# Optimization experiments

Hardware: AMD Instinct MI355X
Metric: run time of the kernel (lower is better)

The kernel has to match this reference:

```python
import jax, jax.numpy as jnp
import numpy as np

N, E, F_IN, HID, OUT, HEADS, NG = 40000, 640000, 64, 128, 64, 4, 64
EPS = 1e-5

def setup_inputs() -> dict:
    key = jax.random.key(0)
    ks = jax.random.split(key, 32)
    d = {}
    d['x'] = jax.random.normal(ks[0], (N, F_IN), dtype=jnp.float32)
    d['edge_index'] = jax.random.randint(ks[1], (2, E), 0, N, dtype=jnp.int64)
    d['batch'] = jnp.sort(jax.random.randint(ks[2], (N,), 0, NG, dtype=jnp.int64))
    fins = [F_IN, HID, HID]
    for i in range(3):
        kk = jax.random.split(ks[3 + i], 6)
        fin = fins[i]
        d[f'W{i}'] = jax.random.normal(kk[0], (fin, HEADS * HID), dtype=jnp.float32) / np.sqrt(fin)
        d[f'as{i}'] = jax.random.normal(kk[1], (HEADS, HID), dtype=jnp.float32) / np.sqrt(HID)
        d[f'ad{i}'] = jax.random.normal(kk[2], (HEADS, HID), dtype=jnp.float32) / np.sqrt(HID)
        d[f'b{i}'] = jnp.zeros((HID,), dtype=jnp.float32)
        d[f'g{i}'] = jnp.ones((HID,), dtype=jnp.float32) + 0.05 * jax.random.normal(kk[3], (HID,), dtype=jnp.float32)
        d[f'be{i}'] = 0.05 * jax.random.normal(kk[4], (HID,), dtype=jnp.float32)
    d['fc1_w'] = jax.random.normal(ks[10], (HID, HID), dtype=jnp.float32) / np.sqrt(HID)
    d['fc1_b'] = jnp.zeros((HID,), dtype=jnp.float32)
    d['fc2_w'] = jax.random.normal(ks[11], (HID, OUT), dtype=jnp.float32) / np.sqrt(HID)
    d['fc2_b'] = jnp.zeros((OUT,), dtype=jnp.float32)
    return d

def _gat(x, src, dst, W, a_s, a_d, b):
    # PyG GATConv, heads=4, concat=False (mean over heads)
    xh = (x @ W).reshape(N, HEADS, HID)            # [N,H,C]
    s_src = jnp.einsum('nhc,hc->nh', xh, a_s)      # [N,H]
    s_dst = jnp.einsum('nhc,hc->nh', xh, a_d)
    e = jax.nn.leaky_relu(s_src[src] + s_dst[dst], 0.2)   # [Etot,H]
    m = jax.ops.segment_max(e, dst, num_segments=N)
    p = jnp.exp(e - m[dst])
    denom = jax.ops.segment_sum(p, dst, num_segments=N)
    alpha = p / denom[dst]                          # segment softmax over dst
    msg = xh[src] * alpha[:, :, None]               # [Etot,H,C]
    out = jax.ops.segment_sum(msg, dst, num_segments=N)  # [N,H,C]
    return out.mean(axis=1) + b

def _bn_eval(x, g, be):
    # running_mean=0, running_var=1 (eval mode)
    return x * (g / jnp.sqrt(1.0 + EPS)) + be

def reference(x, edge_index, batch, W0, as0, ad0, b0, g0, be0, W1, as1, ad1, b1, g1, be1, W2, as2, ad2, b2, g2, be2, fc1_w, fc1_b, fc2_w, fc2_b):
    loop = jnp.arange(N, dtype=edge_index.dtype)
    src = jnp.concatenate([edge_index[0], loop])   # add_self_loops (PyG default)
    dst = jnp.concatenate([edge_index[1], loop])
    h = x
    params = [(W0, as0, ad0, b0, g0, be0), (W1, as1, ad1, b1, g1, be1), (W2, as2, ad2, b2, g2, be2)]
    for (W, a_s, a_d, b, g, be) in params:
        h = _gat(h, src, dst, W, a_s, a_d, b)
        h = jax.nn.relu(_bn_eval(h, g, be))
        # dropout is identity in eval mode
    sums = jax.ops.segment_sum(h, batch, num_segments=NG)
    cnt = jax.ops.segment_sum(jnp.ones((N,), h.dtype), batch, num_segments=NG)
    pooled = sums / jnp.maximum(cnt, 1.0)[:, None]   # global_mean_pool [NG,HID]
    out = jax.nn.relu(pooled @ fc1_w + fc1_b)
    return out @ fc2_w + fc2_b
```

## Files before the change

### kernel.cpp

```cpp
#include <hip/hip_runtime.h>
#include <hip/hip_fp16.h>
#include <math.h>

#define N_NODES 40000
#define N_EDGES 640000
#define FIN 64
#define HID 128
#define OUTDIM 64
#define HEADS 4
#define NGROUPS 64
#define NCOLS 512

typedef _Float16 half8 __attribute__((ext_vector_type(8)));
typedef float f32x4 __attribute__((ext_vector_type(4)));

__device__ __forceinline__ float lrelu(float x) { return x > 0.f ? x : 0.2f * x; }

__device__ __forceinline__ void wave_lds_fence() {
    asm volatile("s_waitcnt lgkmcnt(0)" ::: "memory");
}

#define PREP_X4   (N_NODES * FIN / 4)
#define PREP_WSWZ 20480
#define PREP_V    2560
__global__ void prep_kernel(const float* __restrict__ x, __half* __restrict__ x16,
                            const float* __restrict__ W0, const float* __restrict__ W1,
                            const float* __restrict__ W2,
                            _Float16* __restrict__ F0, _Float16* __restrict__ F1,
                            _Float16* __restrict__ F2,
                            const float* __restrict__ as0, const float* __restrict__ ad0,
                            const float* __restrict__ as1, const float* __restrict__ ad1,
                            const float* __restrict__ as2, const float* __restrict__ ad2,
                            float* __restrict__ v0, float* __restrict__ v1,
                            float* __restrict__ v2) {
    int id = blockIdx.x * 256 + threadIdx.x;
    if (id < PREP_X4) {
        int i4 = id * 4;
        float4 v = *(const float4*)(x + i4);
        __half2 a = __floats2half2_rn(v.x, v.y);
        __half2 b = __floats2half2_rn(v.z, v.w);
        *(__half2*)(x16 + i4)     = a;
        *(__half2*)(x16 + i4 + 2) = b;
        return;
    }
    id -= PREP_X4;
    if (id < PREP_WSWZ) {
        const float* W; _Float16* F; int Kin;
        if (id < 4096)       { W = W0; F = F0; Kin = FIN; }
        else if (id < 12288) { W = W1; F = F1; Kin = HID; id -= 4096; }
        else                 { W = W2; F = F2; Kin = HID; id -= 12288; }
        int KP = Kin * 4;
        int NKg = KP / 32;
        int lane = id & 63;
        int blob = id >> 6;
        int k0g = blob % NKg;
        int cb  = blob / NKg;
        int col = cb * 16 + (lane & 15);
        int kkb = k0g * 32 + (lane >> 4) * 8;
        half8 v;
        #pragma unroll
        for (int e = 0; e < 8; ++e) {
            int kk = kkb + e;
            int k = kk & (Kin - 1);
            int h = kk / Kin;
            v[e] = (_Float16)(0.25f * W[(size_t)k * NCOLS + h * HID + col]);
        }
        *(half8*)(F + (size_t)blob * 512 + lane * 8) = v;
        return;
    }
    id -= PREP_WSWZ;
    if (id < PREP_V) {
        const float* W; const float* as_; const float* ad_; float* v; int j = id;
        if (j < FIN * 8)              { W = W0; as_ = as0; ad_ = ad0; v = v0; }
        else if (j < (FIN + HID) * 8) { W = W1; as_ = as1; ad_ = ad1; v = v1; j -= FIN * 8; }
        else                          { W = W2; as_ = as2; ad_ = ad2; v = v2; j -= (FIN + HID) * 8; }
        int k = j >> 3, sd = (j >> 2) & 1, h = j & 3;
        const float* av = sd ? ad_ : as_;
        float acc = 0.f;
        for (int c = 0; c < HID; ++c)
            acc += W[(size_t)k * NCOLS + h * HID + c] * av[h * HID + c];
        v[k * 8 + sd * 4 + h] = acc;
    }
}

__global__ void deg_count_kernel(const int* __restrict__ ei, int* deg) {
    int e = blockIdx.x * blockDim.x + threadIdx.x;
    if (e < N_EDGES) atomicAdd(&deg[ei[N_EDGES + e]], 1);
}

__global__ void scan1_kernel(const int* __restrict__ deg, int* offsets, int* partial) {
    __shared__ int buf[256];
    int t = threadIdx.x;
    int i = blockIdx.x * 256 + t;
    int v = (i < N_NODES) ? deg[i] + 1 : 0;
    buf[t] = v;
    __syncthreads();
    for (int off = 1; off < 256; off <<= 1) {
        int y = (t >= off) ? buf[t - off] : 0;
        __syncthreads();
        buf[t] += y;
        __syncthreads();
    }
    if (i < N_NODES) offsets[i] = buf[t] - v;
    if (t == 255) partial[blockIdx.x] = buf[255];
}

__global__ void scan2_kernel(int* partial, int nb) {
    __shared__ int buf[256];
    int t = threadIdx.x;
    int v = (t < nb) ? partial[t] : 0;
    buf[t] = v;
    __syncthreads();
    for (int off = 1; off < 256; off <<= 1) {
        int y = (t >= off) ? buf[t - off] : 0;
        __syncthreads();
        buf[t] += y;
        __syncthreads();
    }
    if (t < nb) partial[t] = buf[t] - v;
}

__global__ void scan3_kernel(int* offsets, int* pos, const int* __restrict__ partial) {
    int i = blockIdx.x * 256 + threadIdx.x;
    if (i < N_NODES) {
        int o = offsets[i] + partial[i >> 8];
        offsets[i] = o;
        pos[i] = o;
    }
    if (i == 0) offsets[N_NODES] = N_EDGES + N_NODES;
}

__global__ void scatter_kernel(const int* __restrict__ ei, int* pos, int* csr_src) {
    int i = blockIdx.x * blockDim.x + threadIdx.x;
    if (i < N_EDGES) {
        int s = ei[i];
        int d = ei[N_EDGES + i];
        csr_src[atomicAdd(&pos[d], 1)] = s;
    } else if (i < N_EDGES + N_NODES) {
        int nn = i - N_EDGES;
        csr_src[atomicAdd(&pos[nn], 1)] = nn;
    }
}

template <int K>
__global__ __launch_bounds__(256) void scores3_kernel(const __half* __restrict__ x,
                                                      const float* __restrict__ v,
                                                      float* __restrict__ ssrc,
                                                      float* __restrict__ sdst) {
    __shared__ float vs[K * 8];
    int t = threadIdx.x;
    for (int i = t; i < K * 8; i += 256) vs[i] = v[i];
    __syncthreads();
    int node = blockIdx.x * 256 + t;
    if (node >= N_NODES) return;
    const __half* xr = x + (size_t)node * K;
    f32x4 as = {0.f, 0.f, 0.f, 0.f};
    f32x4 ad = {0.f, 0.f, 0.f, 0.f};
    #pragma unroll 4
    for (int k0 = 0; k0 < K; k0 += 8) {
        uint4 u = *(const uint4*)(xr + k0);
        __half2* hp = (__half2*)&u;
        #pragma unroll
        for (int q = 0; q < 4; ++q) {
            float2 f = __half22float2(hp[q]);
            int k = k0 + 2 * q;
            as += f.x * *(const f32x4*)&vs[k * 8];
            ad += f.x * *(const f32x4*)&vs[k * 8 + 4];
            as += f.y * *(const f32x4*)&vs[(k + 1) * 8];
            ad += f.y * *(const f32x4*)&vs[(k + 1) * 8 + 4];
        }
    }
    *(f32x4*)(ssrc + node * 4) = as;
    *(f32x4*)(sdst + node * 4) = ad;
}

template <int K>
__global__ __launch_bounds__(256) void aggregate_lin_kernel(const __half* __restrict__ tab16,
                                                            const float* __restrict__ s_src,
                                                            const float* __restrict__ s_dst,
                                                            const int* __restrict__ offsets,
                                                            const int* __restrict__ csr_src,
                                                            __half* __restrict__ agg) {
    constexpr int EPR = (K == 128) ? 4 : 8;
    constexpr int LPE = 64 / EPR;
    int wv = threadIdx.x >> 6;
    int lane = threadIdx.x & 63;
    int n = blockIdx.x * 4 + wv;
    if (n >= N_NODES) return;
    int start = offsets[n], end = offsets[n + 1];
    int deg = end - start;
    const float4 sd = *(const float4*)(s_dst + n * 4);
    int cgrp = lane & (LPE - 1);
    int egoff = lane / LPE;

    __shared__ int   roff[4][72];
    __shared__ float al[4][72][4];

    const char* xb = (const char*)tab16 + cgrp * 16;
    float acc[4][8] = {};

    if (lane < 8) {
        roff[wv][64 + lane] = 0;
        *(f32x4*)&al[wv][64 + lane][0] = f32x4{0.f, 0.f, 0.f, 0.f};
    }

    if (deg <= 64) {
        bool act = lane < deg;
        int src = act ? csr_src[start + lane] : 0;
        float4 ss = *(const float4*)(s_src + src * 4);
        float e0 = act ? lrelu(ss.x + sd.x) : -1e30f;
        float e1 = act ? lrelu(ss.y + sd.y) : -1e30f;
        float e2 = act ? lrelu(ss.z + sd.z) : -1e30f;
        float e3 = act ? lrelu(ss.w + sd.w) : -1e30f;
        float m0 = e0, m1 = e1, m2 = e2, m3 = e3;
        #pragma unroll
        for (int o = 32; o > 0; o >>= 1) {
            m0 = fmaxf(m0, __shfl_xor(m0, o));
            m1 = fmaxf(m1, __shfl_xor(m1, o));
            m2 = fmaxf(m2, __shfl_xor(m2, o));
            m3 = fmaxf(m3, __shfl_xor(m3, o));
        }
        float p0 = __expf(e0 - m0), p1 = __expf(e1 - m1);
        float p2 = __expf(e2 - m2), p3 = __expf(e3 - m3);
        float s0 = p0, s1 = p1, s2 = p2, s3 = p3;
        #pragma unroll
        for (int o = 32; o > 0; o >>= 1) {
            s0 += __shfl_xor(s0, o);
            s1 += __shfl_xor(s1, o);
            s2 += __shfl_xor(s2, o);
            s3 += __shfl_xor(s3, o);
        }
        f32x4 av = {p0 / s0, p1 / s1, p2 / s2, p3 / s3};
        roff[wv][lane] = src * (K * 2);
        *(f32x4*)&al[wv][lane][0] = av;
        wave_lds_fence();

        for (int j = 0; j < deg; j += EPR) {
            int eg = j + egoff;
            f32x4 a4 = *(const f32x4*)&al[wv][eg][0];
            uint4 u = *(const uint4*)(xb + roff[wv][eg]);
            __half2* hp = (__half2*)&u;
            #pragma unroll
            for (int q = 0; q < 4; ++q) {
                float2 f = __half22float2(hp[q]);
                #pragma unroll
                for (int h = 0; h < 4; ++h) {
                    acc[h][2 * q]     += a4[h] * f.x;
                    acc[h][2 * q + 1] += a4[h] * f.y;
                }
            }
        }
    } else {
        float m0 = -1e30f, m1 = -1e30f, m2 = -1e30f, m3 = -1e30f;
        for (int j0 = 0; j0 < deg; j0 += 64) {
            int j = j0 + lane;
            bool act = j < deg;
            int src = act ? csr_src[start + j] : 0;
            float4 ss = *(const float4*)(s_src + src * 4);
            m0 = fmaxf(m0, act ? lrelu(ss.x + sd.x) : -1e30f);
            m1 = fmaxf(m1, act ? lrelu(ss.y + sd.y) : -1e30f);
            m2 = fmaxf(m2, act ? lrelu(ss.z + sd.z) : -1e30f);
            m3 = fmaxf(m3, act ? lrelu(ss.w + sd.w) : -1e30f);
        }
        #pragma unroll
        for (int o = 32; o > 0; o >>= 1) {
            m0 = fmaxf(m0, __shfl_xor(m0, o));
            m1 = fmaxf(m1, __shfl_xor(m1, o));
            m2 = fmaxf(m2, __shfl_xor(m2, o));
            m3 = fmaxf(m3, __shfl_xor(m3, o));
        }
        float s0 = 0.f, s1 = 0.f, s2 = 0.f, s3 = 0.f;
        for (int j0 = 0; j0 < deg; j0 += 64) {
            int j = j0 + lane;
            bool act = j < deg;
            int src = act ? csr_src[start + j] : 0;
            float4 ss = *(const float4*)(s_src + src * 4);
            s0 += act ? __expf(lrelu(ss.x + sd.x) - m0) : 0.f;
            s1 += act ? __expf(lrelu(ss.y + sd.y) - m1) : 0.f;
            s2 += act ? __expf(lrelu(ss.z + sd.z) - m2) : 0.f;
            s3 += act ? __expf(lrelu(ss.w + sd.w) - m3) : 0.f;
        }
        #pragma unroll
        for (int o = 32; o > 0; o >>= 1) {
            s0 += __shfl_xor(s0, o);
            s1 += __shfl_xor(s1, o);
            s2 += __shfl_xor(s2, o);
            s3 += __shfl_xor(s3, o);
        }
        float i0 = 1.f / s0, i1 = 1.f / s1, i2 = 1.f / s2, i3 = 1.f / s3;
        for (int j0 = 0; j0 < deg; j0 += 64) {
            int j = j0 + lane;
            bool act = j < deg;
            int src = act ? csr_src[start + j] : 0;
            float4 ss = *(const float4*)(s_src + src * 4);
            f32x4 av;
            av[0] = act ? __expf(lrelu(ss.x + sd.x) - m0) * i0 : 0.f;
            av[1] = act ? __expf(lrelu(ss.y + sd.y) - m1) * i1 : 0.f;
            av[2] = act ? __expf(lrelu(ss.z + sd.z) - m2) * i2 : 0.f;
            av[3] = act ? __expf(lrelu(ss.w + sd.w) - m3) * i3 : 0.f;
            roff[wv][lane] = act ? src * (K * 2) : 0;
            *(f32x4*)&al[wv][lane][0] = av;
            wave_lds_fence();
            int cend = min(64, deg - j0);
            for (int j2 = 0; j2 < cend; j2 += EPR) {
                int eg = j2 + egoff;
                f32x4 a4 = *(const f32x4*)&al[wv][eg][0];
                uint4 u = *(const uint4*)(xb + roff[wv][eg]);
                __half2* hp = (__half2*)&u;
                #pragma unroll
                for (int q = 0; q < 4; ++q) {
                    float2 f = __half22float2(hp[q]);
                    #pragma unroll
                    for (int h = 0; h < 4; ++h) {
                        acc[h][2 * q]     += a4[h] * f.x;
                        acc[h][2 * q + 1] += a4[h] * f.y;
                    }
                }
            }
            wave_lds_fence();
        }
    }

    #pragma unroll
    for (int stride = LPE; stride < 64; stride <<= 1) {
        #pragma unroll
        for (int h = 0; h < 4; ++h)
            #pragma unroll
            for (int r = 0; r < 8; ++r)
                acc[h][r] += __shfl_xor(acc[h][r], stride);
    }
    if (lane < LPE) {
        _Float16* ap = (_Float16*)agg + (size_t)n * (4 * K);
        #pragma unroll
        for (int h = 0; h < 4; ++h) {
            half8 v;
            #pragma unroll
            for (int r = 0; r < 8; ++r) v[r] = (_Float16)acc[h][r];
            *(half8*)(ap + h * K + cgrp * 8) = v;
        }
    }
}

template <int KP, bool SCORES>
__global__ __launch_bounds__(256) void gemm_ep_kernel(const __half* __restrict__ agg,
                                                      const _Float16* __restrict__ Wf,
                                                      const float* __restrict__ bias,
                                                      const float* __restrict__ gamma,
                                                      const float* __restrict__ beta,
                                                      const float* __restrict__ vtab_next,
                                                      __half* __restrict__ h16,
                                                      float* __restrict__ ssrc,
                                                      float* __restrict__ sdst) {
    __shared__ _Float16 As[32][KP + 8];
    __shared__ _Float16 tb[32][136];
    __shared__ float bn_s[3][HID];
    __shared__ float vs[SCORES ? HID * 8 : 8];
    int bm = blockIdx.x * 32;
    int t = threadIdx.x;
    int lane = t & 63;
    int w = t >> 6;
    int wm = w >> 1, wn = w & 1;
    int lr = lane & 15;
    int lk = (lane >> 4) * 8;
    int lg = lane >> 4;

    if (t < HID) {
        bn_s[0][t] = bias[t];
        bn_s[1][t] = gamma[t] * rsqrtf(1.f + 1e-5f);
        bn_s[2][t] = beta[t];
    }
    if (SCORES)
        for (int i = t; i < HID * 8; i += 256) vs[i] = vtab_next[i];
    {
        int row = t >> 3;
        #pragma unroll
        for (int it = 0; it < KP / 64; ++it) {
            int k8 = (t & 7) * 8 + it * 64;
            uint4 av = *(const uint4*)((const _Float16*)agg + (size_t)(bm + row) * KP + k8);
            *(uint4*)&As[row][k8] = av;
        }
    }
    __syncthreads();

    constexpr int NKg = KP / 32;
    f32x4 acc[4] = {};
    #pragma unroll
    for (int k0g = 0; k0g < NKg; ++k0g) {
        half8 af = *(const half8*)&As[wm * 16 + lr][k0g * 32 + lk];
        #pragma unroll
        for (int nn = 0; nn < 4; ++nn) {
            int cb = wn * 4 + nn;
            half8 bf = *(const half8*)(Wf + ((size_t)(cb * NKg + k0g) << 9) + lane * 8);
            acc[nn] = __builtin_amdgcn_mfma_f32_16x16x32_f16(af, bf, acc[nn], 0, 0, 0);
        }
    }

    #pragma unroll
    for (int nn = 0; nn < 4; ++nn) {
        int col = wn * 64 + nn * 16 + lr;
        float b = bn_s[0][col], g = bn_s[1][col], be = bn_s[2][col];
        #pragma unroll
        for (int r = 0; r < 4; ++r) {
            float o = acc[nn][r] + b;
            o = o * g + be;
            tb[wm * 16 + lg * 4 + r][col] = (_Float16)fmaxf(o, 0.f);
        }
    }
    __syncthreads();

    {
        int row = t >> 3;
        int c0 = (t & 7) * 16;
        half8 v0 = *(const half8*)&tb[row][c0];
        half8 v1 = *(const half8*)&tb[row][c0 + 8];
        _Float16* cp = (_Float16*)h16 + (size_t)(bm + row) * HID + c0;
        *(half8*)(cp)     = v0;
        *(half8*)(cp + 8) = v1;
    }

    if (SCORES) {
        int node = t >> 3, j = t & 7;
        float sacc = 0.f;
        #pragma unroll 2
        for (int k0 = 0; k0 < HID; k0 += 8) {
            half8 hv = *(const half8*)&tb[node][k0];
            #pragma unroll
            for (int e = 0; e < 8; ++e)
                sacc += (float)hv[e] * vs[(k0 + e) * 8 + j];
        }
        if (j < 4) ssrc[(bm + node) * 4 + j] = sacc;
        else       sdst[(bm + node) * 4 + (j - 4)] = sacc;
    }
}

__global__ __launch_bounds__(128) void pool_kernel(const __half* __restrict__ h,
                                                   const int* __restrict__ batch,
                                                   float* pooled, float* counts) {
    int t = threadIdx.x;
    int which = t >> 6;
    int c2 = (t & 63) * 2;
    int n0 = blockIdx.x * 256 + which;
    int n1 = min(blockIdx.x * 256 + 256, N_NODES);
    if (n0 >= N_NODES) return;
    int cg = batch[n0];
    float a0 = 0.f, a1 = 0.f, cnt = 0.f;
    for (int n = n0; n < n1; n += 2) {
        int g = batch[n];
        if (g != cg) {
            atomicAdd(&pooled[cg * HID + c2], a0);
            atomicAdd(&pooled[cg * HID + c2 + 1], a1);
            if ((t & 63) == 0) atomicAdd(&counts[cg], cnt);
            a0 = 0.f; a1 = 0.f; cnt = 0.f; cg = g;
        }
        uint u = *(const uint*)(h + (size_t)n * HID + c2);
        __half2 hh = *(__half2*)&u;
        float2 f = __half22float2(hh);
        a0 += f.x; a1 += f.y; cnt += 1.f;
    }
    atomicAdd(&pooled[cg * HID + c2], a0);
    atomicAdd(&pooled[cg * HID + c2 + 1], a1);
    if ((t & 63) == 0) atomicAdd(&counts[cg], cnt);
}

__global__ __launch_bounds__(128) void head_kernel(const float* __restrict__ pooled,
                                                   const float* __restrict__ counts,
                                                   const float* __restrict__ fc1_w,
                                                   const float* __restrict__ fc1_b,
                                                   const float* __restrict__ fc2_w,
                                                   const float* __restrict__ fc2_b,
                                                   float* __restrict__ out) {
    int gI = blockIdx.x;
    int t = threadIdx.x;
    __shared__ float p[HID], hb[HID];
    p[t] = pooled[gI * HID + t] / fmaxf(counts[gI], 1.f);
    __syncthreads();
    float a = fc1_b[t];
    #pragma unroll 4
    for (int k = 0; k < HID; ++k) a += p[k] * fc1_w[k * HID + t];
    hb[t] = fmaxf(a, 0.f);
    __syncthreads();
    if (t < OUTDIM) {
        float o = fc2_b[t];
        #pragma unroll 4
        for (int k = 0; k < HID; ++k) o += hb[k] * fc2_w[k * OUTDIM + t];
        out[gI * OUTDIM + t] = o;
    }
}

extern "C" void kernel_launch(void* const* d_in, const int* in_sizes, int n_in,
                              void* d_out, int out_size, void* d_ws, size_t ws_size,
                              hipStream_t stream) {
    const float* x     = (const float*)d_in[0];
    const int*   ei    = (const int*)d_in[1];
    const int*   batch = (const int*)d_in[2];
    const float* W[3]  = {(const float*)d_in[3],  (const float*)d_in[9],  (const float*)d_in[15]};
    const float* As[3] = {(const float*)d_in[4],  (const float*)d_in[10], (const float*)d_in[16]};
    const float* Ad[3] = {(const float*)d_in[5],  (const float*)d_in[11], (const float*)d_in[17]};
    const float* Bb[3] = {(const float*)d_in[6],  (const float*)d_in[12], (const float*)d_in[18]};
    const float* Gg[3] = {(const float*)d_in[7],  (const float*)d_in[13], (const float*)d_in[19]};
    const float* Be[3] = {(const float*)d_in[8],  (const float*)d_in[14], (const float*)d_in[20]};
    const float* fc1_w = (const float*)d_in[21];
    const float* fc1_b = (const float*)d_in[22];
    const float* fc2_w = (const float*)d_in[23];
    const float* fc2_b = (const float*)d_in[24];

    char* ws = (char*)d_ws;
    size_t off = 0;
    auto alloc = [&](size_t bytes) {
        void* p = ws + off;
        off = (off + bytes + 255) & ~(size_t)255;
        return p;
    };
    __half* agg    = (__half*)alloc((size_t)N_NODES * NCOLS * 2);
    __half* x16    = (__half*)alloc((size_t)N_NODES * FIN * 2);
    __half* h16    = (__half*)alloc((size_t)N_NODES * HID * 2);
    _Float16* Wf[3];
    Wf[0] = (_Float16*)alloc((size_t)(4 * FIN) * HID * 2);
    Wf[1] = (_Float16*)alloc((size_t)(4 * HID) * HID * 2);
    Wf[2] = (_Float16*)alloc((size_t)(4 * HID) * HID * 2);
    float* vtab[3];
    vtab[0] = (float*)alloc((size_t)FIN * 8 * 4);
    vtab[1] = (float*)alloc((size_t)HID * 8 * 4);
    vtab[2] = (float*)alloc((size_t)HID * 8 * 4);
    float* ssrc    = (float*)alloc((size_t)N_NODES * HEADS * 4);
    float* sdst    = (float*)alloc((size_t)N_NODES * HEADS * 4);
    int*   deg     = (int*)alloc((size_t)N_NODES * 4);
    int*   offsets = (int*)alloc((size_t)(N_NODES + 1) * 4);
    int*   pos     = (int*)alloc((size_t)N_NODES * 4);
    int*   partial = (int*)alloc((size_t)256 * 4);
    int*   csr     = (int*)alloc((size_t)(N_EDGES + N_NODES) * 4);
    float* pooled  = (float*)alloc((size_t)NGROUPS * HID * 4 + (size_t)NGROUPS * 4);
    float* counts  = pooled + (size_t)NGROUPS * HID;

    const int PREP_TOTAL = PREP_X4 + PREP_WSWZ + PREP_V;
    prep_kernel<<<(PREP_TOTAL + 255) / 256, 256, 0, stream>>>(
        x, x16, W[0], W[1], W[2], Wf[0], Wf[1], Wf[2],
        As[0], Ad[0], As[1], Ad[1], As[2], Ad[2], vtab[0], vtab[1], vtab[2]);

    const int NB = (N_NODES + 255) / 256;
    hipMemsetAsync(deg, 0, (size_t)N_NODES * 4, stream);
    deg_count_kernel<<<(N_EDGES + 255) / 256, 256, 0, stream>>>(ei, deg);
    scan1_kernel<<<NB, 256, 0, stream>>>(deg, offsets, partial);
    scan2_kernel<<<1, 256, 0, stream>>>(partial, NB);
    scan3_kernel<<<NB, 256, 0, stream>>>(offsets, pos, partial);
    scatter_kernel<<<(N_EDGES + N_NODES + 255) / 256, 256, 0, stream>>>(ei, pos, csr);

    scores3_kernel<64><<<NB, 256, 0, stream>>>(x16, vtab[0], ssrc, sdst);

    aggregate_lin_kernel<64><<<(N_NODES + 3) / 4, 256, 0, stream>>>(
        x16, ssrc, sdst, offsets, csr, agg);
    gemm_ep_kernel<256, true><<<N_NODES / 32, 256, 0, stream>>>(
        agg, Wf[0], Bb[0], Gg[0], Be[0], vtab[1], h16, ssrc, sdst);

    aggregate_lin_kernel<128><<<(N_NODES + 3) / 4, 256, 0, stream>>>(
        h16, ssrc, sdst, offsets, csr, agg);
    gemm_ep_kernel<512, true><<<N_NODES / 32, 256, 0, stream>>>(
        agg, Wf[1], Bb[1], Gg[1], Be[1], vtab[2], h16, ssrc, sdst);

    aggregate_lin_kernel<128><<<(N_NODES + 3) / 4, 256, 0, stream>>>(
        h16, ssrc, sdst, offsets, csr, agg);
    gemm_ep_kernel<512, false><<<N_NODES / 32, 256, 0, stream>>>(
        agg, Wf[2], Bb[2], Gg[2], Be[2], nullptr, h16, nullptr, nullptr);

    hipMemsetAsync(pooled, 0, (size_t)NGROUPS * HID * 4 + (size_t)NGROUPS * 4, stream);
    pool_kernel<<<(N_NODES + 255) / 256, 128, 0, stream>>>(h16, batch, pooled, counts);
    head_kernel<<<NGROUPS, 128, 0, stream>>>(pooled, counts, fc1_w, fc1_b, fc2_w, fc2_b,
                                             (float*)d_out);
}
```

Baseline: 391.4 us.

## Fuse attention aggregation and per-layer GEMM epilogue into one kernel

Merges the aggregate and GEMM+BN+ReLU+scores kernels into a single 512-thread kernel per GAT layer. Each wave aggregates four destination nodes directly into an LDS tile, then the block runs MFMA GEMM on that tile. This removes the global round trip of the 40000x512 fp16 aggregate buffer and one launch per layer. Ping-pong buffers for h and scores avoid read/write hazards between blocks. The trade-off is a larger LDS footprint per block, which may lower occupancy, and the GEMM phase must wait for the slowest wave's gather.

```diff
diff --git a/kernel.cpp b/kernel.cpp
--- a/kernel.cpp
+++ b/kernel.cpp
@@ -174,136 +174,98 @@
     *(f32x4*)(sdst + node * 4) = ad;
 }
 
-template <int K>
-__global__ __launch_bounds__(256) void aggregate_lin_kernel(const __half* __restrict__ tab16,
-                                                            const float* __restrict__ s_src,
-                                                            const float* __restrict__ s_dst,
-                                                            const int* __restrict__ offsets,
-                                                            const int* __restrict__ csr_src,
-                                                            __half* __restrict__ agg) {
+template <int K, bool SCORES>
+__global__ __launch_bounds__(512) void fused_layer_kernel(
+        const __half* __restrict__ tab16,
+        const float* __restrict__ s_src,
+        const float* __restrict__ s_dst,
+        const int* __restrict__ offsets,
+        const int* __restrict__ csr_src,
+        const _Float16* __restrict__ Wf,
+        const float* __restrict__ bias,
+        const float* __restrict__ gamma,
+        const float* __restrict__ beta,
+        const float* __restrict__ vtab_next,
+        __half* __restrict__ h16out,
+        float* __restrict__ ssrc_o,
+        float* __restrict__ sdst_o) {
+    constexpr int KP = 4 * K;
     constexpr int EPR = (K == 128) ? 4 : 8;
     constexpr int LPE = 64 / EPR;
-    int wv = threadIdx.x >> 6;
-    int lane = threadIdx.x & 63;
-    int n = blockIdx.x * 4 + wv;
-    if (n >= N_NODES) return;
-    int start = offsets[n], end = offsets[n + 1];
-    int deg = end - start;
-    const float4 sd = *(const float4*)(s_dst + n * 4);
+    constexpr int NKg = KP / 32;
+
+    __shared__ _Float16 As[32][KP + 8];
+    __shared__ __align__(16) char uali[11520];
+    __shared__ float bn_s[3][HID];
+    __shared__ float vs[SCORES ? HID * 8 : 8];
+
+    int (*roff)[72]    = (int(*)[72])uali;
+    float (*al)[72][4] = (float(*)[72][4])(uali + 8 * 72 * 4);
+    _Float16 (*tb)[136] = (_Float16(*)[136])uali;
+
+    int t = threadIdx.x;
+    int lane = t & 63;
+    int wv = t >> 6;
+    int bm = blockIdx.x * 32;
+
+    if (t < HID) {
+        bn_s[0][t] = bias[t];
+        bn_s[1][t] = gamma[t] * rsqrtf(1.f + 1e-5f);
+        bn_s[2][t] = beta[t];
+    }
+    if (SCORES)
+        for (int i = t; i < HID * 8; i += 512) vs[i] = vtab_next[i];
+
     int cgrp = lane & (LPE - 1);
     int egoff = lane / LPE;
-
-    __shared__ int   roff[4][72];
-    __shared__ float al[4][72][4];
-
     const char* xb = (const char*)tab16 + cgrp * 16;
-    float acc[4][8] = {};
 
     if (lane < 8) {
         roff[wv][64 + lane] = 0;
         *(f32x4*)&al[wv][64 + lane][0] = f32x4{0.f, 0.f, 0.f, 0.f};
     }
 
-    if (deg <= 64) {
-        bool act = lane < deg;
-        int src = act ? csr_src[start + lane] : 0;
-        float4 ss = *(const float4*)(s_src + src * 4);
-        float e0 = act ? lrelu(ss.x + sd.x) : -1e30f;
-        float e1 = act ? lrelu(ss.y + sd.y) : -1e30f;
-        float e2 = act ? lrelu(ss.z + sd.z) : -1e30f;
-        float e3 = act ? lrelu(ss.w + sd.w) : -1e30f;
-        float m0 = e0, m1 = e1, m2 = e2, m3 = e3;
-        #pragma unroll
-        for (int o = 32; o > 0; o >>= 1) {
-            m0 = fmaxf(m0, __shfl_xor(m0, o));
-            m1 = fmaxf(m1, __shfl_xor(m1, o));
-            m2 = fmaxf(m2, __shfl_xor(m2, o));
-            m3 = fmaxf(m3, __shfl_xor(m3, o));
-        }
-        float p0 = __expf(e0 - m0), p1 = __expf(e1 - m1);
-        float p2 = __expf(e2 - m2), p3 = __expf(e3 - m3);
-        float s0 = p0, s1 = p1, s2 = p2, s3 = p3;
-        #pragma unroll
-        for (int o = 32; o > 0; o >>= 1) {
-            s0 += __shfl_xor(s0, o);
-            s1 += __shfl_xor(s1, o);
-            s2 += __shfl_xor(s2, o);
-            s3 += __shfl_xor(s3, o);
-        }
-        f32x4 av = {p0 / s0, p1 / s1, p2 / s2, p3 / s3};
-        roff[wv][lane] = src * (K * 2);
-        *(f32x4*)&al[wv][lane][0] = av;
-        wave_lds_fence();
-
-        for (int j = 0; j < deg; j += EPR) {
-            int eg = j + egoff;
-            f32x4 a4 = *(const f32x4*)&al[wv][eg][0];
-            uint4 u = *(const uint4*)(xb + roff[wv][eg]);
-            __half2* hp = (__half2*)&u;
+    for (int i = 0; i < 4; ++i) {
+        int nl = wv * 4 + i;
+        int n = bm + nl;
+        int start = offsets[n], end = offsets[n + 1];
+        int deg = end - start;
+        const float4 sd = *(const float4*)(s_dst + n * 4);
+        float acc[4][8] = {};
+
+        if (deg <= 64) {
+            bool act = lane < deg;
+            int src = act ? csr_src[start + lane] : 0;
+            float4 ss = *(const float4*)(s_src + src * 4);
+            float e0 = act ? lrelu(ss.x + sd.x) : -1e30f;
+            float e1 = act ? lrelu(ss.y + sd.y) : -1e30f;
+            float e2 = act ? lrelu(ss.z + sd.z) : -1e30f;
+            float e3 = act ? lrelu(ss.w + sd.w) : -1e30f;
+            float m0 = e0, m1 = e1, m2 = e2, m3 = e3;
             #pragma unroll
-            for (int q = 0; q < 4; ++q) {
-                float2 f = __half22float2(hp[q]);
-                #pragma unroll
-                for (int h = 0; h < 4; ++h) {
-                    acc[h][2 * q]     += a4[h] * f.x;
-                    acc[h][2 * q + 1] += a4[h] * f.y;
-                }
-            }
-        }
-    } else {
-        float m0 = -1e30f, m1 = -1e30f, m2 = -1e30f, m3 = -1e30f;
-        for (int j0 = 0; j0 < deg; j0 += 64) {
-            int j = j0 + lane;
-            bool act = j < deg;
-            int src = act ? csr_src[start + j] : 0;
-            float4 ss = *(const float4*)(s_src + src * 4);
-            m0 = fmaxf(m0, act ? lrelu(ss.x + sd.x) : -1e30f);
-            m1 = fmaxf(m1, act ? lrelu(ss.y + sd.y) : -1e30f);
-            m2 = fmaxf(m2, act ? lrelu(ss.z + sd.z) : -1e30f);
-            m3 = fmaxf(m3, act ? lrelu(ss.w + sd.w) : -1e30f);
-        }
-        #pragma unroll
-        for (int o = 32; o > 0; o >>= 1) {
-            m0 = fmaxf(m0, __shfl_xor(m0, o));
-            m1 = fmaxf(m1, __shfl_xor(m1, o));
-            m2 = fmaxf(m2, __shfl_xor(m2, o));
-            m3 = fmaxf(m3, __shfl_xor(m3, o));
-        }
-        float s0 = 0.f, s1 = 0.f, s2 = 0.f, s3 = 0.f;
-        for (int j0 = 0; j0 < deg; j0 += 64) {
-            int j = j0 + lane;
-            bool act = j < deg;
-            int src = act ? csr_src[start + j] : 0;
-            float4 ss = *(const float4*)(s_src + src * 4);
-            s0 += act ? __expf(lrelu(ss.x + sd.x) - m0) : 0.f;
-            s1 += act ? __expf(lrelu(ss.y + sd.y) - m1) : 0.f;
-            s2 += act ? __expf(lrelu(ss.z + sd.z) - m2) : 0.f;
-            s3 += act ? __expf(lrelu(ss.w + sd.w) - m3) : 0.f;
-        }
-        #pragma unroll
-        for (int o = 32; o > 0; o >>= 1) {
-            s0 += __shfl_xor(s0, o);
-            s1 += __shfl_xor(s1, o);
-            s2 += __shfl_xor(s2, o);
-            s3 += __shfl_xor(s3, o);
-        }
-        float i0 = 1.f / s0, i1 = 1.f / s1, i2 = 1.f / s2, i3 = 1.f / s3;
-        for (int j0 = 0; j0 < deg; j0 += 64) {
-            int j = j0 + lane;
-            bool act = j < deg;
-            int src = act ? csr_src[start + j] : 0;
-            float4 ss = *(const float4*)(s_src + src * 4);
-            f32x4 av;
-            av[0] = act ? __expf(lrelu(ss.x + sd.x) - m0) * i0 : 0.f;
-            av[1] = act ? __expf(lrelu(ss.y + sd.y) - m1) * i1 : 0.f;
-            av[2] = act ? __expf(lrelu(ss.z + sd.z) - m2) * i2 : 0.f;
-            av[3] = act ? __expf(lrelu(ss.w + sd.w) - m3) * i3 : 0.f;
-            roff[wv][lane] = act ? src * (K * 2) : 0;
+            for (int o = 32; o > 0; o >>= 1) {
+                m0 = fmaxf(m0, __shfl_xor(m0, o));
+                m1 = fmaxf(m1, __shfl_xor(m1, o));
+                m2 = fmaxf(m2, __shfl_xor(m2, o));
+                m3 = fmaxf(m3, __shfl_xor(m3, o));
+            }
+            float p0 = __expf(e0 - m0), p1 = __expf(e1 - m1);
+            float p2 = __expf(e2 - m2), p3 = __expf(e3 - m3);
+            float s0 = p0, s1 = p1, s2 = p2, s3 = p3;
+            #pragma unroll
+            for (int o = 32; o > 0; o >>= 1) {
+                s0 += __shfl_xor(s0, o);
+                s1 += __shfl_xor(s1, o);
+                s2 += __shfl_xor(s2, o);
+                s3 += __shfl_xor(s3, o);
+            }
+            f32x4 av = {p0 / s0, p1 / s1, p2 / s2, p3 / s3};
+            roff[wv][lane] = src * (K * 2);
             *(f32x4*)&al[wv][lane][0] = av;
             wave_lds_fence();
-            int cend = min(64, deg - j0);
-            for (int j2 = 0; j2 < cend; j2 += EPR) {
-                int eg = j2 + egoff;
+
+            for (int j = 0; j < deg; j += EPR) {
+                int eg = j + egoff;
                 f32x4 a4 = *(const f32x4*)&al[wv][eg][0];
                 uint4 u = *(const uint4*)(xb + roff[wv][eg]);
                 __half2* hp = (__half2*)&u;
@@ -317,91 +279,121 @@
                     }
                 }
             }
-            wave_lds_fence();
-        }
-    }
-
-    #pragma unroll
-    for (int stride = LPE; stride < 64; stride <<= 1) {
+        } else {
+            float m0 = -1e30f, m1 = -1e30f, m2 = -1e30f, m3 = -1e30f;
+            for (int j0 = 0; j0 < deg; j0 += 64) {
+                int j = j0 + lane;
+                bool act = j < deg;
+                int src = act ? csr_src[start + j] : 0;
+                float4 ss = *(const float4*)(s_src + src * 4);
+                m0 = fmaxf(m0, act ? lrelu(ss.x + sd.x) : -1e30f);
+                m1 = fmaxf(m1, act ? lrelu(ss.y + sd.y) : -1e30f);
+                m2 = fmaxf(m2, act ? lrelu(ss.z + sd.z) : -1e30f);
+                m3 = fmaxf(m3, act ? lrelu(ss.w + sd.w) : -1e30f);
+            }
+            #pragma unroll
+            for (int o = 32; o > 0; o >>= 1) {
+                m0 = fmaxf(m0, __shfl_xor(m0, o));
+                m1 = fmaxf(m1, __shfl_xor(m1, o));
+                m2 = fmaxf(m2, __shfl_xor(m2, o));
+                m3 = fmaxf(m3, __shfl_xor(m3, o));
+            }
+            float s0 = 0.f, s1 = 0.f, s2 = 0.f, s3 = 0.f;
+            for (int j0 = 0; j0 < deg; j0 += 64) {
+                int j = j0 + lane;
+                bool act = j < deg;
+                int src = act ? csr_src[start + j] : 0;
+                float4 ss = *(const float4*)(s_src + src * 4);
+                s0 += act ? __expf(lrelu(ss.x + sd.x) - m0) : 0.f;
+                s1 += act ? __expf(lrelu(ss.y + sd.y) - m1) : 0.f;
+                s2 += act ? __expf(lrelu(ss.z + sd.z) - m2) : 0.f;
+                s3 += act ? __expf(lrelu(ss.w + sd.w) - m3) : 0.f;
+            }
+            #pragma unroll
+            for (int o = 32; o > 0; o >>= 1) {
+                s0 += __shfl_xor(s0, o);
+                s1 += __shfl_xor(s1, o);
+                s2 += __shfl_xor(s2, o);
+                s3 += __shfl_xor(s3, o);
+            }
+            float i0 = 1.f / s0, i1 = 1.f / s1, i2 = 1.f / s2, i3 = 1.f / s3;
+            for (int j0 = 0; j0 < deg; j0 += 64) {
+                int j = j0 + lane;
+                bool act = j < deg;
+                int src = act ? csr_src[start + j] : 0;
+                float4 ss = *(const float4*)(s_src + src * 4);
+                f32x4 av;
+                av[0] = act ? __expf(lrelu(ss.x + sd.x) - m0) * i0 : 0.f;
+                av[1] = act ? __expf(lrelu(ss.y + sd.y) - m1) * i1 : 0.f;
+                av[2] = act ? __expf(lrelu(ss.z + sd.z) - m2) * i2 : 0.f;
+                av[3] = act ? __expf(lrelu(ss.w + sd.w) - m3) * i3 : 0.f;
+                roff[wv][lane] = act ? src * (K * 2) : 0;
+                *(f32x4*)&al[wv][lane][0] = av;
+                wave_lds_fence();
+                int cend = min(64, deg - j0);
+                for (int j2 = 0; j2 < cend; j2 += EPR) {
+                    int eg = j2 + egoff;
+                    f32x4 a4 = *(const f32x4*)&al[wv][eg][0];
+                    uint4 u = *(const uint4*)(xb + roff[wv][eg]);
+                    __half2* hp = (__half2*)&u;
+                    #pragma unroll
+                    for (int q = 0; q < 4; ++q) {
+                        float2 f = __half22float2(hp[q]);
+                        #pragma unroll
+                        for (int h = 0; h < 4; ++h) {
+                            acc[h][2 * q]     += a4[h] * f.x;
+                            acc[h][2 * q + 1] += a4[h] * f.y;
+                        }
+                    }
+                }
+                wave_lds_fence();
+            }
+        }
+
         #pragma unroll
-        for (int h = 0; h < 4; ++h)
+        for (int stride = LPE; stride < 64; stride <<= 1) {
             #pragma unroll
-            for (int r = 0; r < 8; ++r)
-                acc[h][r] += __shfl_xor(acc[h][r], stride);
-    }
-    if (lane < LPE) {
-        _Float16* ap = (_Float16*)agg + (size_t)n * (4 * K);
-        #pragma unroll
-        for (int h = 0; h < 4; ++h) {
-            half8 v;
+            for (int h = 0; h < 4; ++h)
+                #pragma unroll
+                for (int r = 0; r < 8; ++r)
+                    acc[h][r] += __shfl_xor(acc[h][r], stride);
+        }
+        if (lane < LPE) {
             #pragma unroll
-            for (int r = 0; r < 8; ++r) v[r] = (_Float16)acc[h][r];
-            *(half8*)(ap + h * K + cgrp * 8) = v;
-        }
-    }
-}
-
-template <int KP, bool SCORES>
-__global__ __launch_bounds__(256) void gemm_ep_kernel(const __half* __restrict__ agg,
-                                                      const _Float16* __restrict__ Wf,
-                                                      const float* __restrict__ bias,
-                                                      const float* __restrict__ gamma,
-                                                      const float* __restrict__ beta,
-                                                      const float* __restrict__ vtab_next,
-                                                      __half* __restrict__ h16,
-                                                      float* __restrict__ ssrc,
-                                                      float* __restrict__ sdst) {
-    __shared__ _Float16 As[32][KP + 8];
-    __shared__ _Float16 tb[32][136];
-    __shared__ float bn_s[3][HID];
-    __shared__ float vs[SCORES ? HID * 8 : 8];
-    int bm = blockIdx.x * 32;
-    int t = threadIdx.x;
-    int lane = t & 63;
-    int w = t >> 6;
-    int wm = w >> 1, wn = w & 1;
+            for (int h = 0; h < 4; ++h) {
+                half8 v;
+                #pragma unroll
+                for (int r = 0; r < 8; ++r) v[r] = (_Float16)acc[h][r];
+                *(half8*)&As[nl][h * K + cgrp * 8] = v;
+            }
+        }
+        wave_lds_fence();
+    }
+    __syncthreads();
+
+    int wm = wv >> 2, wn = wv & 3;
     int lr = lane & 15;
     int lk = (lane >> 4) * 8;
     int lg = lane >> 4;
-
-    if (t < HID) {
-        bn_s[0][t] = bias[t];
-        bn_s[1][t] = gamma[t] * rsqrtf(1.f + 1e-5f);
-        bn_s[2][t] = beta[t];
-    }
-    if (SCORES)
-        for (int i = t; i < HID * 8; i += 256) vs[i] = vtab_next[i];
-    {
-        int row = t >> 3;
-        #pragma unroll
-        for (int it = 0; it < KP / 64; ++it) {
-            int k8 = (t & 7) * 8 + it * 64;
-            uint4 av = *(const uint4*)((const _Float16*)agg + (size_t)(bm + row) * KP + k8);
-            *(uint4*)&As[row][k8] = av;
-        }
-    }
-    __syncthreads();
-
-    constexpr int NKg = KP / 32;
-    f32x4 acc[4] = {};
+    f32x4 acc2[2] = {};
     #pragma unroll
     for (int k0g = 0; k0g < NKg; ++k0g) {
         half8 af = *(const half8*)&As[wm * 16 + lr][k0g * 32 + lk];
         #pragma unroll
-        for (int nn = 0; nn < 4; ++nn) {
-            int cb = wn * 4 + nn;
+        for (int nn = 0; nn < 2; ++nn) {
+            int cb = wn * 2 + nn;
             half8 bf = *(const half8*)(Wf + ((size_t)(cb * NKg + k0g) << 9) + lane * 8);
-            acc[nn] = __builtin_amdgcn_mfma_f32_16x16x32_f16(af, bf, acc[nn], 0, 0, 0);
+            acc2[nn] = __builtin_amdgcn_mfma_f32_16x16x32_f16(af, bf, acc2[nn], 0, 0, 0);
         }
     }
 
     #pragma unroll
-    for (int nn = 0; nn < 4; ++nn) {
-        int col = wn * 64 + nn * 16 + lr;
+    for (int nn = 0; nn < 2; ++nn) {
+        int col = wn * 32 + nn * 16 + lr;
         float b = bn_s[0][col], g = bn_s[1][col], be = bn_s[2][col];
         #pragma unroll
         for (int r = 0; r < 4; ++r) {
-            float o = acc[nn][r] + b;
+            float o = acc2[nn][r] + b;
             o = o * g + be;
             tb[wm * 16 + lg * 4 + r][col] = (_Float16)fmaxf(o, 0.f);
         }
@@ -409,27 +401,26 @@
     __syncthreads();
 
     {
-        int row = t >> 3;
-        int c0 = (t & 7) * 16;
+        int row = t >> 4;
+        int c0 = (t & 15) * 8;
         half8 v0 = *(const half8*)&tb[row][c0];
-        half8 v1 = *(const half8*)&tb[row][c0 + 8];
-        _Float16* cp = (_Float16*)h16 + (size_t)(bm + row) * HID + c0;
-        *(half8*)(cp)     = v0;
-        *(half8*)(cp + 8) = v1;
+        *(half8*)((_Float16*)h16out + (size_t)(bm + row) * HID + c0) = v0;
     }
 
     if (SCORES) {
-        int node = t >> 3, j = t & 7;
-        float sacc = 0.f;
-        #pragma unroll 2
-        for (int k0 = 0; k0 < HID; k0 += 8) {
-            half8 hv = *(const half8*)&tb[node][k0];
-            #pragma unroll
-            for (int e = 0; e < 8; ++e)
-                sacc += (float)hv[e] * vs[(k0 + e) * 8 + j];
-        }
-        if (j < 4) ssrc[(bm + node) * 4 + j] = sacc;
-        else       sdst[(bm + node) * 4 + (j - 4)] = sacc;
+        if (t < 256) {
+            int node = t >> 3, j = t & 7;
+            float sacc = 0.f;
+            #pragma unroll 2
+            for (int k0 = 0; k0 < HID; k0 += 8) {
+                half8 hv = *(const half8*)&tb[node][k0];
+                #pragma unroll
+                for (int e = 0; e < 8; ++e)
+                    sacc += (float)hv[e] * vs[(k0 + e) * 8 + j];
+            }
+            if (j < 4) ssrc_o[(bm + node) * 4 + j] = sacc;
+            else       sdst_o[(bm + node) * 4 + (j - 4)] = sacc;
+        }
     }
 }
 
@@ -494,7 +485,7 @@
     const int*   ei    = (const int*)d_in[1];
     const int*   batch = (const int*)d_in[2];
     const float* W[3]  = {(const float*)d_in[3],  (const float*)d_in[9],  (const float*)d_in[15]};
-    const float* As[3] = {(const float*)d_in[4],  (const float*)d_in[10], (const float*)d_in[16]};
+    const float* As_[3] = {(const float*)d_in[4],  (const float*)d_in[10], (const float*)d_in[16]};
     const float* Ad[3] = {(const float*)d_in[5],  (const float*)d_in[11], (const float*)d_in[17]};
     const float* Bb[3] = {(const float*)d_in[6],  (const float*)d_in[12], (const float*)d_in[18]};
     const float* Gg[3] = {(const float*)d_in[7],  (const float*)d_in[13], (const float*)d_in[19]};
@@ -511,9 +502,9 @@
         off = (off + bytes + 255) & ~(size_t)255;
         return p;
     };
-    __half* agg    = (__half*)alloc((size_t)N_NODES * NCOLS * 2);
     __half* x16    = (__half*)alloc((size_t)N_NODES * FIN * 2);
-    __half* h16    = (__half*)alloc((size_t)N_NODES * HID * 2);
+    __half* h16A   = (__half*)alloc((size_t)N_NODES * HID * 2);
+    __half* h16B   = (__half*)alloc((size_t)N_NODES * HID * 2);
     _Float16* Wf[3];
     Wf[0] = (_Float16*)alloc((size_t)(4 * FIN) * HID * 2);
     Wf[1] = (_Float16*)alloc((size_t)(4 * HID) * HID * 2);
@@ -522,8 +513,10 @@
     vtab[0] = (float*)alloc((size_t)FIN * 8 * 4);
     vtab[1] = (float*)alloc((size_t)HID * 8 * 4);
     vtab[2] = (float*)alloc((size_t)HID * 8 * 4);
-    float* ssrc    = (float*)alloc((size_t)N_NODES * HEADS * 4);
-    float* sdst    = (float*)alloc((size_t)N_NODES * HEADS * 4);
+    float* ssrcA   = (float*)alloc((size_t)N_NODES * HEADS * 4);
+    float* sdstA   = (float*)alloc((size_t)N_NODES * HEADS * 4);
+    float* ssrcB   = (float*)alloc((size_t)N_NODES * HEADS * 4);
+    float* sdstB   = (float*)alloc((size_t)N_NODES * HEADS * 4);
     int*   deg     = (int*)alloc((size_t)N_NODES * 4);
     int*   offsets = (int*)alloc((size_t)(N_NODES + 1) * 4);
     int*   pos     = (int*)alloc((size_t)N_NODES * 4);
@@ -535,7 +528,7 @@
     const int PREP_TOTAL = PREP_X4 + PREP_WSWZ + PREP_V;
     prep_kernel<<<(PREP_TOTAL + 255) / 256, 256, 0, stream>>>(
         x, x16, W[0], W[1], W[2], Wf[0], Wf[1], Wf[2],
-        As[0], Ad[0], As[1], Ad[1], As[2], Ad[2], vtab[0], vtab[1], vtab[2]);
+        As_[0], Ad[0], As_[1], Ad[1], As_[2], Ad[2], vtab[0], vtab[1], vtab[2]);
 
     const int NB = (N_NODES + 255) / 256;
     hipMemsetAsync(deg, 0, (size_t)N_NODES * 4, stream);
@@ -545,25 +538,20 @@
     scan3_kernel<<<NB, 256, 0, stream>>>(offsets, pos, partial);
     scatter_kernel<<<(N_EDGES + N_NODES + 255) / 256, 256, 0, stream>>>(ei, pos, csr);
 
-    scores3_kernel<64><<<NB, 256, 0, stream>>>(x16, vtab[0], ssrc, sdst);
-
-    aggregate_lin_kernel<64><<<(N_NODES + 3) / 4, 256, 0, stream>>>(
-        x16, ssrc, sdst, offsets, csr, agg);
-    gemm_ep_kernel<256, true><<<N_NODES / 32, 256, 0, stream>>>(
-        agg, Wf[0], Bb[0], Gg[0], Be[0], vtab[1], h16, ssrc, sdst);
-
-    aggregate_lin_kernel<128><<<(N_NODES + 3) / 4, 256, 0, stream>>>(
-        h16, ssrc, sdst, offsets, csr, agg);
-    gemm_ep_kernel<512, true><<<N_NODES / 32, 256, 0, stream>>>(
-        agg, Wf[1], Bb[1], Gg[1], Be[1], vtab[2], h16, ssrc, sdst);
-
-    aggregate_lin_kernel<128><<<(N_NODES + 3) / 4, 256, 0, stream>>>(
-        h16, ssrc, sdst, offsets, csr, agg);
-    gemm_ep_kernel<512, false><<<N_NODES / 32, 256, 0, stream>>>(
-        agg, Wf[2], Bb[2], Gg[2], Be[2], nullptr, h16, nullptr, nullptr);
+    scores3_kernel<64><<<NB, 256, 0, stream>>>(x16, vtab[0], ssrcA, sdstA);
+
+    fused_layer_kernel<64, true><<<N_NODES / 32, 512, 0, stream>>>(
+        x16, ssrcA, sdstA, offsets, csr, Wf[0], Bb[0], Gg[0], Be[0],
+        vtab[1], h16A, ssrcB, sdstB);
+    fused_layer_kernel<128, true><<<N_NODES / 32, 512, 0, stream>>>(
+        h16A, ssrcB, sdstB, offsets, csr, Wf[1], Bb[1], Gg[1], Be[1],
+        vtab[2], h16B, ssrcA, sdstA);
+    fused_layer_kernel<128, false><<<N_NODES / 32, 512, 0, stream>>>(
+        h16B, ssrcA, sdstA, offsets, csr, Wf[2], Bb[2], Gg[2], Be[2],
+        nullptr, h16A, nullptr, nullptr);
 
     hipMemsetAsync(pooled, 0, (size_t)NGROUPS * HID * 4 + (size_t)NGROUPS * 4, stream);
-    pool_kernel<<<(N_NODES + 255) / 256, 128, 0, stream>>>(h16, batch, pooled, counts);
+    pool_kernel<<<(N_NODES + 255) / 256, 128, 0, stream>>>(h16A, batch, pooled, counts);
     head_kernel<<<NGROUPS, 128, 0, stream>>>(pooled, counts, fc1_w, fc1_b, fc2_w, fc2_b,
                                              (float*)d_out);
 }
```

Measured after the change: 394.0 us. About the same (+0.6%).
